# Kernel optimization log

Measured on AMD Instinct MI355X. Metric: run time of the kernel, lower is better.

## Reference

```python
import jax, jax.numpy as jnp
import numpy as np

QMIN, QMAX = -128.0, 127.0
SMALL_SCALE_THRESHOLD = 6.1e-05


def quant_kernel(x):
    # x: [M, K] float32 -> per-row scale (f32), zero point (i32), precomputed sum (i32), q (i8)
    rmin = jnp.minimum(jnp.min(x, axis=1), 0.0).astype(jnp.float32)
    rmax = jnp.maximum(jnp.max(x, axis=1), 0.0).astype(jnp.float32)
    scale = (rmax - rmin) / (QMAX - QMIN)
    # faithful replication of `scale == 0.0 + isinf(1/scale)` (precedence: 0.0 + bool)
    isinf = jnp.isinf(1.0 / scale)
    scale = jnp.where(scale == (0.0 + isinf.astype(jnp.float32)), 0.1, scale)
    small = scale < SMALL_SCALE_THRESHOLD
    amp = SMALL_SCALE_THRESHOLD / scale
    scale = jnp.where(small, SMALL_SCALE_THRESHOLD, scale)
    rmax = jnp.where(small, amp * rmax, rmax)
    rmin = jnp.where(small, amp * rmin, rmin)
    zp_from_min = QMIN - rmin / scale
    zp_from_max = QMAX - rmax / scale
    err_min = abs(QMIN) + jnp.abs(rmin / scale)
    err_max = abs(QMAX) + jnp.abs(rmax / scale)
    zp0 = jnp.where(err_min < err_max, zp_from_min, zp_from_max)
    zp = jnp.round(zp0).astype(jnp.int32)
    zp = jnp.where(zp0 < QMIN, jnp.int32(QMIN), zp)
    zp = jnp.where(zp0 > QMAX, jnp.int32(QMAX), zp)
    inv = 1.0 / scale
    sums = jnp.round(jnp.sum(x, axis=1) * inv).astype(jnp.int32)
    t = jnp.round(x * inv[:, None]) + zp[:, None].astype(jnp.float32)
    q = jnp.clip(t, QMIN, QMAX).astype(jnp.int8)
    return scale, zp, sums, q


def dequant_kernel(d, bias, m1_scales, m1_zeros, m1_sums, m2_scales, m2_zeros, m2_sums):
    # d: [M, N] int32 raw GEMM; m1_*: [M, 1]; m2_*: [1, N]
    temp = (m1_zeros * m2_sums).astype(jnp.int32) + (m1_sums * m2_zeros).astype(jnp.int32)
    scale = m1_scales * m2_scales
    return bias + ((d - temp).astype(jnp.float32) * scale).astype(bias.dtype)


def setup_inputs() -> dict:
    key = jax.random.key(0)
    k1, k2, k3, k4, k5 = jax.random.split(key, 5)
    B, S, K, N = 4, 4096, 1024, 1024
    inp = jax.random.normal(k1, (B, S, K), dtype=jnp.float32)
    qweight = jax.random.randint(k2, (N, K), -128, 128, dtype=jnp.int32).astype(jnp.int8)
    bias = jax.random.normal(k3, (N,), dtype=jnp.float32)
    w_scales = (jax.random.uniform(k4, (N,), dtype=jnp.float32) * 0.01 + 1e-3)
    w_zeros = jax.random.randint(k5, (N,), -10, 10, dtype=jnp.int32)
    # consistent precomputed weight sums (sum of quantized vals minus K*zero)
    w_sums = (jnp.sum(qweight.astype(jnp.int32), axis=1) - K * w_zeros).astype(jnp.int32)
    return {"inp": inp, "qweight": qweight, "bias": bias,
            "w_scales": w_scales, "w_zeros": w_zeros, "w_sums": w_sums}


def reference(inp, qweight, bias, w_scales, w_zeros, w_sums):
    B, S, K = inp.shape
    x = inp.reshape(B * S, K)
    scales, zeros, sums, qinp = quant_kernel(x)
    # int8 GEMM accumulated in int32: [M, K] @ [K, N]
    d = jnp.matmul(qinp.astype(jnp.int32), qweight.T.astype(jnp.int32))
    M, N = d.shape
    out = dequant_kernel(d, bias, scales.reshape(M, 1), zeros.reshape(M, 1),
                         sums.reshape(M, 1), w_scales.reshape(1, N),
                         w_zeros.reshape(1, N), w_sums.reshape(1, N))
    return out.reshape(B, S, N)
```

## Files before the change

### kernel.cpp

```cpp
#include <hip/hip_runtime.h>
#include <cstdint>
#include <cstddef>

typedef int v4i __attribute__((ext_vector_type(4)));

#define QMIN_F (-128.0f)
#define QMAX_F (127.0f)
#define SMALL_THR 6.1e-05f

#define WAITVM(n) asm volatile("s_waitcnt vmcnt(" #n ")" ::: "memory")
#define WAITLGKM0 asm volatile("s_waitcnt lgkmcnt(0)" ::: "memory")

__global__ __launch_bounds__(256) void quant_rows_kernel(
    const float* __restrict__ x, signed char* __restrict__ q,
    float* __restrict__ scales, int* __restrict__ zps, int* __restrict__ sums,
    const int* __restrict__ w32, int* __restrict__ w8pk, int n4, int K) {
  const int gidx = blockIdx.x * 256 + threadIdx.x;
  if (gidx < n4) {
    v4i pv = *(const v4i*)(w32 + gidx * 4);
    w8pk[gidx] = (pv.x & 255) | ((pv.y & 255) << 8) | ((pv.z & 255) << 16) |
                 (pv.w << 24);
  }

  const int wave = threadIdx.x >> 6;
  const int lane = threadIdx.x & 63;
  const int row  = blockIdx.x * 4 + wave;
  const float* xr = x + (size_t)row * K;

  float4 v[4];
  float vmin = 0.0f, vmax = 0.0f, vsum = 0.0f;
#pragma unroll
  for (int j = 0; j < 4; ++j) {
    v[j] = *(const float4*)(xr + j * 256 + lane * 4);
    vmin = fminf(vmin, fminf(fminf(v[j].x, v[j].y), fminf(v[j].z, v[j].w)));
    vmax = fmaxf(vmax, fmaxf(fmaxf(v[j].x, v[j].y), fmaxf(v[j].z, v[j].w)));
    vsum += (v[j].x + v[j].y) + (v[j].z + v[j].w);
  }
#pragma unroll
  for (int off = 32; off >= 1; off >>= 1) {
    vmin = fminf(vmin, __shfl_xor(vmin, off));
    vmax = fmaxf(vmax, __shfl_xor(vmax, off));
    vsum += __shfl_xor(vsum, off);
  }

  float scale = (vmax - vmin) / (QMAX_F - QMIN_F);
  float isinf_f = isinf(1.0f / scale) ? 1.0f : 0.0f;
  if (scale == isinf_f) scale = 0.1f;
  float rmin = vmin, rmax = vmax;
  if (scale < SMALL_THR) {
    float amp = SMALL_THR / scale;
    scale = SMALL_THR;
    rmax *= amp;
    rmin *= amp;
  }
  float rdmin = rmin / scale, rdmax = rmax / scale;
  float err_min = 128.0f + fabsf(rdmin);
  float err_max = 127.0f + fabsf(rdmax);
  float zp0 = (err_min < err_max) ? (QMIN_F - rdmin) : (QMAX_F - rdmax);
  int zp = (int)rintf(zp0);
  if (zp0 < QMIN_F) zp = -128;
  if (zp0 > QMAX_F) zp = 127;
  float inv = 1.0f / scale;

  if (lane == 0) {
    scales[row] = scale;
    zps[row]    = zp;
    sums[row]   = (int)rintf(vsum * inv);
  }

  const float zpf = (float)zp;
  int* qi = (int*)(q + (size_t)row * K);
#pragma unroll
  for (int j = 0; j < 4; ++j) {
    float t0 = fminf(fmaxf(rintf(v[j].x * inv) + zpf, QMIN_F), QMAX_F);
    float t1 = fminf(fmaxf(rintf(v[j].y * inv) + zpf, QMIN_F), QMAX_F);
    float t2 = fminf(fmaxf(rintf(v[j].z * inv) + zpf, QMIN_F), QMAX_F);
    float t3 = fminf(fmaxf(rintf(v[j].w * inv) + zpf, QMIN_F), QMAX_F);
    int pack = ((int)t0 & 255) | (((int)t1 & 255) << 8) |
               (((int)t2 & 255) << 16) | ((int)t3 << 24);
    qi[j * 64 + lane] = pack;
  }
}

__device__ __forceinline__ void gload_lds16(const void* g, void* l) {
  __builtin_amdgcn_global_load_lds(
      (const __attribute__((address_space(1))) void*)g,
      (__attribute__((address_space(3))) void*)l, 16, 0, 0);
}

#define BUFA_SZ 16384
#define BUFB_SZ 8192

__device__ __forceinline__ void stage_tile(
    const signed char* __restrict__ q, const signed char* __restrict__ w,
    char* buf, int rowA0, int rowB0, int k0, int K, int tid) {
#pragma unroll
  for (int i = 0; i < 4; ++i) {
    int c  = (i << 8) + tid;
    int r  = c >> 2;
    int sl = (c & 3) ^ ((r >> 1) & 3);
    gload_lds16(q + (size_t)(rowA0 + r) * K + k0 + (sl << 4), buf + (c << 4));
  }
#pragma unroll
  for (int i = 0; i < 2; ++i) {
    int c  = (i << 8) + tid;
    int r  = c >> 2;
    int sl = (c & 3) ^ ((r >> 1) & 3);
    gload_lds16(w + (size_t)(rowB0 + r) * K + k0 + (sl << 4),
                buf + BUFA_SZ + (c << 4));
  }
}

__global__ __launch_bounds__(256, 2) void gemm_dequant_kernel(
    const signed char* __restrict__ q, const signed char* __restrict__ w,
    const float* __restrict__ scales, const int* __restrict__ zps,
    const int* __restrict__ sums, const float* __restrict__ bias,
    const float* __restrict__ w_scales, const int* __restrict__ w_zeros,
    const int* __restrict__ w_sums, float* __restrict__ out,
    int N, int K, int nblk) {
  __shared__ char sh[2][BUFA_SZ + BUFB_SZ];
  const int tid  = threadIdx.x;
  const int lane = tid & 63;
  const int wave = tid >> 6;
  const int wr = wave >> 1;
  const int wc = wave & 1;
  const int fr = lane & 15;
  const int kb = lane >> 4;
  const int ntN = N >> 7;
  const int per = nblk >> 3;
  const int lin = ((int)blockIdx.x & 7) * per + ((int)blockIdx.x >> 3);
  const int rowA0 = (lin / ntN) << 8;
  const int rowB0 = (lin % ntN) << 7;
  const int wrbase = wr << 7;
  const int wcbase = wc << 6;

  v4i acc[8][4];
#pragma unroll
  for (int i = 0; i < 8; ++i)
#pragma unroll
    for (int j = 0; j < 4; ++j) {
      v4i z = {0, 0, 0, 0};
      acc[i][j] = z;
    }

  const int NT = K >> 6;
  stage_tile(q, w, sh[0], rowA0, rowB0, 0, K, tid);

  for (int t = 0; t < NT; ++t) {
    if (t + 1 < NT) {
      stage_tile(q, w, sh[(t + 1) & 1], rowA0, rowB0, (t + 1) << 6, K, tid);
      WAITVM(6);
    } else {
      WAITVM(0);
    }
    __builtin_amdgcn_s_barrier();

    const char* bA = sh[t & 1];
    const char* bB = bA + BUFA_SZ;

    v4i afrag[8], bfrag[4];
#pragma unroll
    for (int n = 0; n < 4; ++n) {
      int rb = wcbase + (n << 4) + fr;
      bfrag[n] = *(const v4i*)(bB + (rb << 6) + ((kb ^ ((rb >> 1) & 3)) << 4));
    }
#pragma unroll
    for (int m = 0; m < 8; ++m) {
      int ra = wrbase + (m << 4) + fr;
      afrag[m] = *(const v4i*)(bA + (ra << 6) + ((kb ^ ((ra >> 1) & 3)) << 4));
    }
    WAITLGKM0;
    __builtin_amdgcn_s_barrier();

    __builtin_amdgcn_s_setprio(1);
#pragma unroll
    for (int m = 0; m < 8; ++m)
#pragma unroll
      for (int n = 0; n < 4; ++n)
        acc[m][n] = __builtin_amdgcn_mfma_i32_16x16x64_i8(afrag[m], bfrag[n],
                                                          acc[m][n], 0, 0, 0);
    __builtin_amdgcn_s_setprio(0);
  }

  const int baseM = rowA0 + wrbase;
  const int baseN = rowB0 + wcbase;
  const int qr = (lane >> 4) << 2;
  const int qc = lane & 15;
  float cb[4], cwsc[4];
  int cwz[4], cws[4];
#pragma unroll
  for (int n = 0; n < 4; ++n) {
    int col = baseN + (n << 4) + qc;
    cb[n]   = bias[col];
    cwsc[n] = w_scales[col];
    cwz[n]  = w_zeros[col];
    cws[n]  = w_sums[col];
  }
#pragma unroll
  for (int i = 0; i < 8; ++i) {
    const int m0 = baseM + (i << 4) + qr;
    float sc[4];
    int zp4[4], sm4[4];
#pragma unroll
    for (int j = 0; j < 4; ++j) {
      sc[j]  = scales[m0 + j];
      zp4[j] = zps[m0 + j];
      sm4[j] = sums[m0 + j];
    }
#pragma unroll
    for (int n = 0; n < 4; ++n) {
      const int col = baseN + (n << 4) + qc;
#pragma unroll
      for (int j = 0; j < 4; ++j) {
        int d    = acc[i][n][j];
        int temp = zp4[j] * cws[n] + sm4[j] * cwz[n];
        out[(size_t)(m0 + j) * N + col] =
            cb[n] + (float)(d - temp) * (sc[j] * cwsc[n]);
      }
    }
  }
}

extern "C" void kernel_launch(void* const* d_in, const int* in_sizes, int n_in,
                              void* d_out, int out_size, void* d_ws, size_t ws_size,
                              hipStream_t stream) {
  const float* inp      = (const float*)d_in[0];
  const int*   qw32     = (const int*)d_in[1];
  const float* bias     = (const float*)d_in[2];
  const float* w_scales = (const float*)d_in[3];
  const int*   w_zeros  = (const int*)d_in[4];
  const int*   w_sums   = (const int*)d_in[5];

  const int N = in_sizes[2];
  const int K = in_sizes[1] / N;
  const int M = in_sizes[0] / K;

  float*       scales = (float*)d_ws;
  int*         zps    = (int*)((char*)d_ws + (size_t)M * 4);
  int*         sums   = (int*)((char*)d_ws + (size_t)M * 8);
  signed char* q      = (signed char*)((char*)d_ws + (size_t)M * 12);
  signed char* w8     = (signed char*)((char*)d_ws + (size_t)M * 12 + (size_t)M * K);

  const int n4 = (N * K) / 4;
  const int nblk = (M / 256) * (N / 128);
  quant_rows_kernel<<<M / 4, 256, 0, stream>>>(inp, q, scales, zps, sums,
                                               qw32, (int*)w8, n4, K);
  gemm_dequant_kernel<<<nblk, 256, 0, stream>>>(
      q, w8, scales, zps, sums, bias, w_scales, w_zeros, w_sums,
      (float*)d_out, N, K, nblk);
}
```

Measured before the change: 47.32 us.

## Use 8-wave GEMM blocks with interleaved LDS reads and MFMA scheduling

Result: no change. 46.53 us (-1.7%).

```diff
diff --git a/kernel.cpp b/kernel.cpp
--- a/kernel.cpp
+++ b/kernel.cpp
@@ -9,7 +9,7 @@
 #define SMALL_THR 6.1e-05f
 
 #define WAITVM(n) asm volatile("s_waitcnt vmcnt(" #n ")" ::: "memory")
-#define WAITLGKM0 asm volatile("s_waitcnt lgkmcnt(0)" ::: "memory")
+#define SCHEDBAR __builtin_amdgcn_sched_barrier(0)
 
 __global__ __launch_bounds__(256) void quant_rows_kernel(
     const float* __restrict__ x, signed char* __restrict__ q,
@@ -95,15 +95,14 @@
     const signed char* __restrict__ q, const signed char* __restrict__ w,
     char* buf, int rowA0, int rowB0, int k0, int K, int tid) {
 #pragma unroll
-  for (int i = 0; i < 4; ++i) {
-    int c  = (i << 8) + tid;
+  for (int i = 0; i < 2; ++i) {
+    int c  = (i << 9) + tid;
     int r  = c >> 2;
     int sl = (c & 3) ^ ((r >> 1) & 3);
     gload_lds16(q + (size_t)(rowA0 + r) * K + k0 + (sl << 4), buf + (c << 4));
   }
-#pragma unroll
-  for (int i = 0; i < 2; ++i) {
-    int c  = (i << 8) + tid;
+  {
+    int c  = tid;
     int r  = c >> 2;
     int sl = (c & 3) ^ ((r >> 1) & 3);
     gload_lds16(w + (size_t)(rowB0 + r) * K + k0 + (sl << 4),
@@ -111,7 +110,11 @@
   }
 }
 
-__global__ __launch_bounds__(256, 2) void gemm_dequant_kernel(
+__device__ __forceinline__ v4i lds_frag(const char* base, int row, int kb) {
+  return *(const v4i*)(base + (row << 6) + ((kb ^ ((row >> 1) & 3)) << 4));
+}
+
+__global__ __launch_bounds__(512, 4) void gemm_dequant_kernel(
     const signed char* __restrict__ q, const signed char* __restrict__ w,
     const float* __restrict__ scales, const int* __restrict__ zps,
     const int* __restrict__ sums, const float* __restrict__ bias,
@@ -122,8 +125,8 @@
   const int tid  = threadIdx.x;
   const int lane = tid & 63;
   const int wave = tid >> 6;
-  const int wr = wave >> 1;
-  const int wc = wave & 1;
+  const int wrbase = (wave >> 1) << 6;
+  const int wcbase = (wave & 1) << 6;
   const int fr = lane & 15;
   const int kb = lane >> 4;
   const int ntN = N >> 7;
@@ -131,12 +134,10 @@
   const int lin = ((int)blockIdx.x & 7) * per + ((int)blockIdx.x >> 3);
   const int rowA0 = (lin / ntN) << 8;
   const int rowB0 = (lin % ntN) << 7;
-  const int wrbase = wr << 7;
-  const int wcbase = wc << 6;
-
-  v4i acc[8][4];
-#pragma unroll
-  for (int i = 0; i < 8; ++i)
+
+  v4i acc[4][4];
+#pragma unroll
+  for (int i = 0; i < 4; ++i)
 #pragma unroll
     for (int j = 0; j < 4; ++j) {
       v4i z = {0, 0, 0, 0};
@@ -145,41 +146,53 @@
 
   const int NT = K >> 6;
   stage_tile(q, w, sh[0], rowA0, rowB0, 0, K, tid);
+  stage_tile(q, w, sh[1], rowA0, rowB0, 64, K, tid);
 
   for (int t = 0; t < NT; ++t) {
-    if (t + 1 < NT) {
-      stage_tile(q, w, sh[(t + 1) & 1], rowA0, rowB0, (t + 1) << 6, K, tid);
-      WAITVM(6);
-    } else {
-      WAITVM(0);
-    }
+    if (t + 1 < NT) { WAITVM(3); } else { WAITVM(0); }
     __builtin_amdgcn_s_barrier();
 
     const char* bA = sh[t & 1];
     const char* bB = bA + BUFA_SZ;
 
-    v4i afrag[8], bfrag[4];
-#pragma unroll
-    for (int n = 0; n < 4; ++n) {
-      int rb = wcbase + (n << 4) + fr;
-      bfrag[n] = *(const v4i*)(bB + (rb << 6) + ((kb ^ ((rb >> 1) & 3)) << 4));
-    }
-#pragma unroll
-    for (int m = 0; m < 8; ++m) {
-      int ra = wrbase + (m << 4) + fr;
-      afrag[m] = *(const v4i*)(bA + (ra << 6) + ((kb ^ ((ra >> 1) & 3)) << 4));
-    }
-    WAITLGKM0;
+    v4i af0 = lds_frag(bA, wrbase + 0  + fr, kb);
+    v4i af1 = lds_frag(bA, wrbase + 16 + fr, kb);
+    v4i bf0 = lds_frag(bB, wcbase + 0  + fr, kb);
+    v4i bf1 = lds_frag(bB, wcbase + 16 + fr, kb);
+    SCHEDBAR;
+    v4i bf2 = lds_frag(bB, wcbase + 32 + fr, kb);
+    v4i bf3 = lds_frag(bB, wcbase + 48 + fr, kb);
+    __builtin_amdgcn_s_setprio(1);
+    acc[0][0] = __builtin_amdgcn_mfma_i32_16x16x64_i8(af0, bf0, acc[0][0], 0, 0, 0);
+    acc[0][1] = __builtin_amdgcn_mfma_i32_16x16x64_i8(af0, bf1, acc[0][1], 0, 0, 0);
+    acc[1][0] = __builtin_amdgcn_mfma_i32_16x16x64_i8(af1, bf0, acc[1][0], 0, 0, 0);
+    acc[1][1] = __builtin_amdgcn_mfma_i32_16x16x64_i8(af1, bf1, acc[1][1], 0, 0, 0);
+    __builtin_amdgcn_s_setprio(0);
+    SCHEDBAR;
+    v4i af2 = lds_frag(bA, wrbase + 32 + fr, kb);
+    v4i af3 = lds_frag(bA, wrbase + 48 + fr, kb);
+    __builtin_amdgcn_s_setprio(1);
+    acc[0][2] = __builtin_amdgcn_mfma_i32_16x16x64_i8(af0, bf2, acc[0][2], 0, 0, 0);
+    acc[0][3] = __builtin_amdgcn_mfma_i32_16x16x64_i8(af0, bf3, acc[0][3], 0, 0, 0);
+    acc[1][2] = __builtin_amdgcn_mfma_i32_16x16x64_i8(af1, bf2, acc[1][2], 0, 0, 0);
+    acc[1][3] = __builtin_amdgcn_mfma_i32_16x16x64_i8(af1, bf3, acc[1][3], 0, 0, 0);
+    __builtin_amdgcn_s_setprio(0);
+    SCHEDBAR;
+    __builtin_amdgcn_s_setprio(1);
+    acc[2][0] = __builtin_amdgcn_mfma_i32_16x16x64_i8(af2, bf0, acc[2][0], 0, 0, 0);
+    acc[2][1] = __builtin_amdgcn_mfma_i32_16x16x64_i8(af2, bf1, acc[2][1], 0, 0, 0);
+    acc[3][0] = __builtin_amdgcn_mfma_i32_16x16x64_i8(af3, bf0, acc[3][0], 0, 0, 0);
+    acc[3][1] = __builtin_amdgcn_mfma_i32_16x16x64_i8(af3, bf1, acc[3][1], 0, 0, 0);
+    acc[2][2] = __builtin_amdgcn_mfma_i32_16x16x64_i8(af2, bf2, acc[2][2], 0, 0, 0);
+    acc[2][3] = __builtin_amdgcn_mfma_i32_16x16x64_i8(af2, bf3, acc[2][3], 0, 0, 0);
+    acc[3][2] = __builtin_amdgcn_mfma_i32_16x16x64_i8(af3, bf2, acc[3][2], 0, 0, 0);
+    acc[3][3] = __builtin_amdgcn_mfma_i32_16x16x64_i8(af3, bf3, acc[3][3], 0, 0, 0);
+    __builtin_amdgcn_s_setprio(0);
+    SCHEDBAR;
+
     __builtin_amdgcn_s_barrier();
-
-    __builtin_amdgcn_s_setprio(1);
-#pragma unroll
-    for (int m = 0; m < 8; ++m)
-#pragma unroll
-      for (int n = 0; n < 4; ++n)
-        acc[m][n] = __builtin_amdgcn_mfma_i32_16x16x64_i8(afrag[m], bfrag[n],
-                                                          acc[m][n], 0, 0, 0);
-    __builtin_amdgcn_s_setprio(0);
+    if (t + 2 < NT)
+      stage_tile(q, w, sh[t & 1], rowA0, rowB0, (t + 2) << 6, K, tid);
   }
 
   const int baseM = rowA0 + wrbase;
@@ -197,7 +210,7 @@
     cws[n]  = w_sums[col];
   }
 #pragma unroll
-  for (int i = 0; i < 8; ++i) {
+  for (int i = 0; i < 4; ++i) {
     const int m0 = baseM + (i << 4) + qr;
     float sc[4];
     int zp4[4], sm4[4];
@@ -245,7 +258,7 @@
   const int nblk = (M / 256) * (N / 128);
   quant_rows_kernel<<<M / 4, 256, 0, stream>>>(inp, q, scales, zps, sums,
                                                qw32, (int*)w8, n4, K);
-  gemm_dequant_kernel<<<nblk, 256, 0, stream>>>(
+  gemm_dequant_kernel<<<nblk, 512, 0, stream>>>(
       q, w8, scales, zps, sums, bias, w_scales, w_zeros, w_sums,
       (float*)d_out, N, K, nblk);
 }
```
